# Kernel tuning notes

Measured on AMD Instinct MI355X. Metric: run time of the kernel, lower is better.

The kernel has to match this reference:

```python
import jax, jax.numpy as jnp
import numpy as np
from jax import lax

NPOINTS = 4096
K = 16
BN_EPS = 1e-5


def _fps_idx(pts, npoints):
    """Farthest point sampling indices for one cloud. pts: [N,3] -> [npoints] int32."""
    N = pts.shape[0]

    def body(carry, _):
        dist, last = carry
        d = jnp.sum((pts - pts[last]) ** 2, axis=-1)  # [N]
        dist = jnp.minimum(dist, d)
        nxt = jnp.argmax(dist).astype(jnp.int32)
        return (dist, nxt), nxt

    init = (jnp.full((N,), 1e10, pts.dtype), jnp.array(0, jnp.int32))
    _, rest = lax.scan(body, init, None, length=npoints - 1)
    return jnp.concatenate([jnp.zeros((1,), jnp.int32), rest])


def setup_inputs() -> dict:
    key = jax.random.key(0)
    k1, k2, k3 = jax.random.split(key, 3)
    B, N = 4, 16384
    P, Q = 64, 128
    return {
        "xyz": jax.random.normal(k1, (B, N, 3), jnp.float32),
        "w_planes": jax.random.normal(k2, (P, 3), jnp.float32) * 0.1,   # Conv2d(3->P,1x1,no bias)
        "w_shapes": jax.random.normal(k3, (Q, P), jnp.float32) * 0.1,   # Conv1d(P->Q,1,no bias)
        "bn_gamma": jnp.ones((Q,), jnp.float32),
        "bn_beta": jnp.zeros((Q,), jnp.float32),
        "bn_mean": jnp.zeros((Q,), jnp.float32),
        "bn_var": jnp.ones((Q,), jnp.float32),
    }


def reference(xyz, w_planes, w_shapes, bn_gamma, bn_beta, bn_mean, bn_var):
    # xyz: [B, N, 3]
    # 1) FPS -> xyz_new [B, S, 3]
    fps_idx = jax.vmap(lambda p: _fps_idx(p, NPOINTS))(xyz)            # [B, S]
    xyz_new = jnp.take_along_axis(xyz, fps_idx[:, :, None], axis=1)    # [B, S, 3]

    # 2) KNN of xyz_new in xyz (squared-L2, ascending)
    d = (jnp.sum(xyz_new ** 2, -1)[:, :, None]
         + jnp.sum(xyz ** 2, -1)[:, None, :]
         - 2.0 * jnp.einsum('bsc,bnc->bsn', xyz_new, xyz))             # [B, S, N]
    _, idx = lax.top_k(-d, K)                                          # [B, S, K], nearest first
    idx_nb = idx[:, :, 1:]                                             # drop self -> [B, S, K-1]

    # 3) group_points + center: relative neighbor coords
    knn = jax.vmap(lambda p, i: p[i])(xyz, idx_nb)                     # [B, S, K-1, 3]
    rel = knn - xyz_new[:, :, None, :]                                 # [B, S, K-1, 3]
    nrm = jnp.linalg.norm(rel, axis=-1, keepdims=True) + 1e-8          # [B, S, K-1, 1]

    # 4) 1x1 conv over coords, normalize, weighted max over neighbors
    planes = jnp.einsum('bskc,pc->bskp', rel, w_planes) / nrm          # [B, S, K-1, P]
    planes = jnp.max(nrm * planes * jnp.abs(planes), axis=2)           # [B, S, P]

    # 5) MLP: Conv1d(no bias) + BatchNorm1d(eval) + ReLU
    x = jnp.einsum('bsp,qp->bsq', planes, w_shapes)                    # [B, S, Q]
    x = (x - bn_mean) * (bn_gamma / jnp.sqrt(bn_var + BN_EPS)) + bn_beta
    shapes = jax.nn.relu(x).transpose(0, 2, 1)                         # [B, Q, S]
    return shapes, xyz_new, idx
```

## Files before the change

kernel.cpp:

```cpp
#include <hip/hip_runtime.h>

#define BB 4
#define NN 16384
#define SS 4096
#define KK 16
#define KE 17
#define PP 64
#define QQ 128

#define OFF_XYZNEW 2097152u
#define OFF_IDX    2146304u
#define OUT_ELEMS  2408448u

#define FTH 512
#define FPT (NN / FTH)
#define PAIRS (FPT / 2)
#define NWAVE (FTH / 64)

#define KTH 64
#define NBLK (SS / KTH)
#define CAP 32
#define UU  16
#define MARGIN 1e-3f

typedef float float2v __attribute__((ext_vector_type(2)));

__device__ __forceinline__ float mulrn(float a, float b) { return __fmul_rn(a, b); }
__device__ __forceinline__ float addrn(float a, float b) { return __fadd_rn(a, b); }
__device__ __forceinline__ float subrn(float a, float b) { return __fsub_rn(a, b); }

template<int CTRL>
__device__ __forceinline__ void dpp_amax(float& bv, int& bg)
{
    int vi = __builtin_amdgcn_update_dpp(__float_as_int(bv), __float_as_int(bv),
                                         CTRL, 0xf, 0xf, false);
    int gi = __builtin_amdgcn_update_dpp(bg, bg, CTRL, 0xf, 0xf, false);
    float ov = __int_as_float(vi);
    bool c = (ov > bv) | ((ov == bv) & (gi < bg));
    bg = c ? gi : bg;
    bv = c ? ov : bv;
}

__global__ __launch_bounds__(FTH)
__attribute__((amdgpu_waves_per_eu(2, 2)))
void fps_kernel(
    const float* __restrict__ xyz,
    float* __restrict__ out,
    float* __restrict__ ws, unsigned ws_floats)
{
    const int b   = blockIdx.x;
    const int tid = threadIdx.x;
    const float* base = xyz + (size_t)b * NN * 3;

    float2v pxx[PAIRS], pyy[PAIRS], pzz[PAIRS], pdd[PAIRS];
#pragma unroll
    for (int i = 0; i < PAIRS; ++i) {
        int g0 = tid + FTH * (2 * i);
        int g1 = tid + FTH * (2 * i + 1);
        pxx[i] = (float2v){ base[g0 * 3 + 0], base[g1 * 3 + 0] };
        pyy[i] = (float2v){ base[g0 * 3 + 1], base[g1 * 3 + 1] };
        pzz[i] = (float2v){ base[g0 * 3 + 2], base[g1 * 3 + 2] };
        pdd[i] = (float2v){ 1e10f, 1e10f };
        asm volatile("" : "+v"(pxx[i]));
        asm volatile("" : "+v"(pyy[i]));
        asm volatile("" : "+v"(pzz[i]));
    }

    __shared__ uint2 wvg[2][NWAVE];

    float lx = base[0], ly = base[1], lz = base[2];
    if (tid == 0) {
        unsigned o = OFF_XYZNEW + (unsigned)b * SS * 3u;
        out[o + 0] = lx; out[o + 1] = ly; out[o + 2] = lz;
        unsigned w = (unsigned)b * SS * 3u;
        if (w + 2u < ws_floats) { ws[w] = lx; ws[w + 1] = ly; ws[w + 2] = lz; }
    }

    const int lane = tid & 63;
    const int wave = tid >> 6;
    int p = 0;

    for (int s = 1; s < SS; ++s) {
#pragma clang fp contract(off)
        const float2v lx2 = (float2v){ lx, lx };
        const float2v ly2 = (float2v){ ly, ly };
        const float2v lz2 = (float2v){ lz, lz };
        float bestv = -1.0f;
        int   bestg = 0;
#pragma unroll
        for (int i = 0; i < PAIRS; ++i) {
            float2v dx = pxx[i] - lx2;
            float2v dy = pyy[i] - ly2;
            float2v dz = pzz[i] - lz2;
            float2v dd = (dx * dx + dy * dy) + dz * dz;
            float n0 = fminf(pdd[i].x, dd.x);
            float n1 = fminf(pdd[i].y, dd.y);
            pdd[i] = (float2v){ n0, n1 };
            bestg = (n0 > bestv) ? (tid + FTH * (2 * i)) : bestg;
            bestv = fmaxf(bestv, n0);
            bestg = (n1 > bestv) ? (tid + FTH * (2 * i + 1)) : bestg;
            bestv = fmaxf(bestv, n1);
        }

        dpp_amax<0x111>(bestv, bestg);
        dpp_amax<0x112>(bestv, bestg);
        dpp_amax<0x114>(bestv, bestg);
        dpp_amax<0x118>(bestv, bestg);
        dpp_amax<0x142>(bestv, bestg);
        dpp_amax<0x143>(bestv, bestg);

        if (lane == 63) wvg[p][wave] = make_uint2(__float_as_uint(bestv), (unsigned)bestg);
        __syncthreads();

        uint2 e0 = wvg[p][0];
        float bv = __uint_as_float(e0.x); int bg = (int)e0.y;
#pragma unroll
        for (int w = 1; w < NWAVE; ++w) {
            uint2 e = wvg[p][w];
            float v = __uint_as_float(e.x); int g = (int)e.y;
            bool c = (v > bv) | ((v == bv) & (g < bg));
            bg = c ? g : bg;
            bv = c ? v : bv;
        }

        int bgu = __builtin_amdgcn_readfirstlane(bg);
        lx = base[bgu * 3 + 0];
        ly = base[bgu * 3 + 1];
        lz = base[bgu * 3 + 2];

        if (tid == 0) {
            unsigned o = OFF_XYZNEW + ((unsigned)b * SS + (unsigned)s) * 3u;
            out[o + 0] = lx; out[o + 1] = ly; out[o + 2] = lz;
            unsigned w = ((unsigned)b * SS + (unsigned)s) * 3u;
            if (w + 2u < ws_floats) { ws[w] = lx; ws[w + 1] = ly; ws[w + 2] = lz; }
        }
        p ^= 1;
    }
}

__global__ __launch_bounds__(KTH) void knn_shape_kernel(
    const float* __restrict__ xyz,
    const float* __restrict__ ws, int use_ws, unsigned ws_floats,
    const float* __restrict__ w_planes, const float* __restrict__ w_shapes,
    const float* __restrict__ bn_gamma, const float* __restrict__ bn_beta,
    const float* __restrict__ bn_mean, const float* __restrict__ bn_var,
    float* __restrict__ out)
{
    __shared__ float sd[CAP][KTH];
    __shared__ int   sg[CAP][KTH];
    __shared__ float wpx[PP], wpy[PP], wpz[PP];
    __shared__ float wsh[QQ * PP];
    __shared__ float bsc[QQ], bmn[QQ], bbt[QQ];

    const int tid = threadIdx.x;
    const int blk = blockIdx.x;
    const int b   = blk / NBLK;
    const int s   = (blk % NBLK) * KTH + tid;

    for (int i = tid; i < PP; i += KTH) {
        wpx[i] = w_planes[i * 3 + 0];
        wpy[i] = w_planes[i * 3 + 1];
        wpz[i] = w_planes[i * 3 + 2];
    }
    for (int i = tid; i < QQ * PP; i += KTH) wsh[i] = w_shapes[i];
    for (int i = tid; i < QQ; i += KTH) {
        bsc[i] = bn_gamma[i] / sqrtf(bn_var[i] + 1e-5f);
        bmn[i] = bn_mean[i];
        bbt[i] = bn_beta[i];
    }
    __syncthreads();

    const float* bx = xyz + (size_t)b * NN * 3;

    float qx, qy, qz;
    {
        unsigned w = ((unsigned)b * SS + (unsigned)s) * 3u;
        if (use_ws && w + 2u < ws_floats) {
            qx = ws[w]; qy = ws[w + 1]; qz = ws[w + 2];
        } else {
            unsigned o = OFF_XYZNEW + w;
            qx = out[o + 0]; qy = out[o + 1]; qz = out[o + 2];
        }
    }
    const float  qsq   = addrn(addrn(mulrn(qx, qx), mulrn(qy, qy)), mulrn(qz, qz));
    const double qxd = (double)qx, qyd = (double)qy, qzd = (double)qz;
    const double qsq64 = qxd * qxd + qyd * qyd + qzd * qzd;

    float  kd[KE];   int ki[KE];
    double kd64[KK]; int ki64[KK];
#pragma unroll
    for (int t = 0; t < KE; ++t) { kd[t] = 3.0e38f; ki[t] = 0; }
#pragma unroll
    for (int t = 0; t < KK; ++t) { kd64[t] = 1.0e300; ki64[t] = 0; }

    int   cnt  = 0;
    float taum = 3.0e38f;

    auto drain = [&]() {
        for (int t = 0; t < CAP; ++t) {
            if (!__any(t < cnt)) break;
            const bool act = t < cnt;
            float d = 0.0f; int g = 0;
            if (act) { d = sd[t][tid]; g = sg[t][tid]; }
            if (act) {
                if (d < kd[KE - 1]) {
                    kd[KE - 1] = d; ki[KE - 1] = g;
#pragma unroll
                    for (int t2 = KE - 1; t2 >= 1; --t2) {
                        if (kd[t2] < kd[t2 - 1]) {
                            float td = kd[t2]; kd[t2] = kd[t2 - 1]; kd[t2 - 1] = td;
                            int   ti = ki[t2]; ki[t2] = ki[t2 - 1]; ki[t2 - 1] = ti;
                        }
                    }
                }
                const float* pg = bx + (size_t)g * 3u;
                float x = pg[0], y = pg[1], z = pg[2];
                double xd = (double)x, yd = (double)y, zd = (double)z;
                double tq64  = xd * xd + yd * yd + zd * zd;
                double dot64 = xd * qxd + yd * qyd + zd * qzd;
                double d64   = qsq64 + tq64 - 2.0 * dot64;
                if (d64 < kd64[KK - 1]) {
                    kd64[KK - 1] = d64; ki64[KK - 1] = g;
#pragma unroll
                    for (int t2 = KK - 1; t2 >= 1; --t2) {
                        if (kd64[t2] < kd64[t2 - 1]) {
                            double td = kd64[t2]; kd64[t2] = kd64[t2 - 1]; kd64[t2 - 1] = td;
                            int    ti = ki64[t2]; ki64[t2] = ki64[t2 - 1]; ki64[t2 - 1] = ti;
                        }
                    }
                }
            }
        }
        cnt  = 0;
        taum = kd[KE - 1] + MARGIN;
    };

    for (int g0 = 0; g0 < NN; g0 += UU) {
        float4 c4[12];
        const float4* p4 = reinterpret_cast<const float4*>(bx + (size_t)g0 * 3u);
#pragma unroll
        for (int i = 0; i < 12; ++i) c4[i] = p4[i];
        const float* cf = reinterpret_cast<const float*>(c4);
#pragma unroll
        for (int u = 0; u < UU; ++u) {
            int g = g0 + u;
            float x = cf[u * 3 + 0];
            float y = cf[u * 3 + 1];
            float z = cf[u * 3 + 2];
            float tq  = addrn(addrn(mulrn(x, x), mulrn(y, y)), mulrn(z, z));
            float dot = fmaf(z, qz, fmaf(y, qy, mulrn(x, qx)));
            float d   = subrn(addrn(qsq, tq), mulrn(2.0f, dot));
            if (d < taum) { sd[cnt][tid] = d; sg[cnt][tid] = g; ++cnt; }
        }
        if (__any(cnt > CAP - UU)) drain();
    }
    drain();

    bool agree = true;
#pragma unroll
    for (int t = 0; t < KK; ++t) agree = agree && (ki[t] == ki64[t]);

    bool hastie = false;
#pragma unroll
    for (int t = 1; t < KE; ++t) hastie = hastie || (kd[t] == kd[t - 1]);

    const bool use_f32 = agree || hastie;
    int kf[KK];
#pragma unroll
    for (int t = 0; t < KK; ++t) kf[t] = use_f32 ? ki[t] : ki64[t];

    float pl[PP];
#pragma unroll
    for (int p = 0; p < PP; ++p) pl[p] = -3.0e38f;

    for (int k = 1; k < KK; ++k) {
        int g = kf[k];
        float rx = bx[g * 3 + 0] - qx;
        float ry = bx[g * 3 + 1] - qy;
        float rz = bx[g * 3 + 2] - qz;
        float nrm  = sqrtf(rx * rx + ry * ry + rz * rz) + 1e-8f;
        float invn = 1.0f / nrm;
        for (int p = 0; p < PP; ++p) {
            float t = rx * wpx[p] + ry * wpy[p] + rz * wpz[p];
            float a = t * invn;
            float v = nrm * a * fabsf(a);
            pl[p] = fmaxf(pl[p], v);
        }
    }

    for (int q = 0; q < QQ; ++q) {
        float acc = 0.0f;
        for (int p = 0; p < PP; ++p) acc = fmaf(pl[p], wsh[q * PP + p], acc);
        float y2 = (acc - bmn[q]) * bsc[q] + bbt[q];
        y2 = fmaxf(y2, 0.0f);
        unsigned o = ((unsigned)b * QQ + (unsigned)q) * SS + (unsigned)s;
        out[o] = y2;
    }

    for (int t = 0; t < KK; ++t) {
        unsigned o = OFF_IDX + ((unsigned)b * SS + (unsigned)s) * (unsigned)KK + (unsigned)t;
        out[o] = (float)kf[t];
    }
}

extern "C" void kernel_launch(void* const* d_in, const int* in_sizes, int n_in,
                              void* d_out, int out_size, void* d_ws, size_t ws_size,
                              hipStream_t stream)
{
    const float* xyz      = (const float*)d_in[0];
    const float* w_planes = (const float*)d_in[1];
    const float* w_shapes = (const float*)d_in[2];
    const float* bn_gamma = (const float*)d_in[3];
    const float* bn_beta  = (const float*)d_in[4];
    const float* bn_mean  = (const float*)d_in[5];
    const float* bn_var   = (const float*)d_in[6];

    float* out = (float*)d_out;
    float* ws  = (float*)d_ws;

    const unsigned ws_floats = (unsigned)(ws_size / 4);
    const int use_ws = (ws_size >= (size_t)BB * SS * 3 * 4) ? 1 : 0;

    hipLaunchKernelGGL(fps_kernel, dim3(BB), dim3(FTH), 0, stream,
                       xyz, out, ws, ws_floats);

    hipLaunchKernelGGL(knn_shape_kernel, dim3(BB * NBLK), dim3(KTH), 0, stream,
                       xyz, ws, use_ws, ws_floats,
                       w_planes, w_shapes,
                       bn_gamma, bn_beta, bn_mean, bn_var,
                       out);
}
```

Baseline: 8.000 ms.

## Split KNN candidate scan across four waves per query block and merge

```diff
diff --git a/kernel.cpp b/kernel.cpp
--- a/kernel.cpp
+++ b/kernel.cpp
@@ -17,10 +17,13 @@
 #define PAIRS (FPT / 2)
 #define NWAVE (FTH / 64)
 
-#define KTH 64
-#define NBLK (SS / KTH)
-#define CAP 32
-#define UU  16
+#define KTH 256
+#define NW 4
+#define PART (NN / NW)
+#define QPB 64
+#define NBLK (SS / QPB)
+#define CAP 12
+#define UU  8
 #define MARGIN 1e-3f
 
 typedef float float2v __attribute__((ext_vector_type(2)));
@@ -149,20 +152,22 @@
     __shared__ float sd[CAP][KTH];
     __shared__ int   sg[CAP][KTH];
     __shared__ float wpx[PP], wpy[PP], wpz[PP];
-    __shared__ float wsh[QQ * PP];
     __shared__ float bsc[QQ], bmn[QQ], bbt[QQ];
-
-    const int tid = threadIdx.x;
-    const int blk = blockIdx.x;
-    const int b   = blk / NBLK;
-    const int s   = (blk % NBLK) * KTH + tid;
+    __shared__ int   ski[NW][KE][QPB];
+    __shared__ int   ski64[NW][KK][QPB];
+
+    const int tid  = threadIdx.x;
+    const int lane = tid & 63;
+    const int w    = tid >> 6;
+    const int blk  = blockIdx.x;
+    const int b    = blk / NBLK;
+    const int s    = (blk % NBLK) * QPB + lane;
 
     for (int i = tid; i < PP; i += KTH) {
         wpx[i] = w_planes[i * 3 + 0];
         wpy[i] = w_planes[i * 3 + 1];
         wpz[i] = w_planes[i * 3 + 2];
     }
-    for (int i = tid; i < QQ * PP; i += KTH) wsh[i] = w_shapes[i];
     for (int i = tid; i < QQ; i += KTH) {
         bsc[i] = bn_gamma[i] / sqrtf(bn_var[i] + 1e-5f);
         bmn[i] = bn_mean[i];
@@ -174,11 +179,11 @@
 
     float qx, qy, qz;
     {
-        unsigned w = ((unsigned)b * SS + (unsigned)s) * 3u;
-        if (use_ws && w + 2u < ws_floats) {
-            qx = ws[w]; qy = ws[w + 1]; qz = ws[w + 2];
+        unsigned wq = ((unsigned)b * SS + (unsigned)s) * 3u;
+        if (use_ws && wq + 2u < ws_floats) {
+            qx = ws[wq]; qy = ws[wq + 1]; qz = ws[wq + 2];
         } else {
-            unsigned o = OFF_XYZNEW + w;
+            unsigned o = OFF_XYZNEW + wq;
             qx = out[o + 0]; qy = out[o + 1]; qz = out[o + 2];
         }
     }
@@ -235,11 +240,12 @@
         taum = kd[KE - 1] + MARGIN;
     };
 
-    for (int g0 = 0; g0 < NN; g0 += UU) {
-        float4 c4[12];
+    const int gbeg = w * PART;
+    for (int g0 = gbeg; g0 < gbeg + PART; g0 += UU) {
+        float4 c4[6];
         const float4* p4 = reinterpret_cast<const float4*>(bx + (size_t)g0 * 3u);
 #pragma unroll
-        for (int i = 0; i < 12; ++i) c4[i] = p4[i];
+        for (int i = 0; i < 6; ++i) c4[i] = p4[i];
         const float* cf = reinterpret_cast<const float*>(c4);
 #pragma unroll
         for (int u = 0; u < UU; ++u) {
@@ -256,50 +262,124 @@
     }
     drain();
 
-    bool agree = true;
-#pragma unroll
-    for (int t = 0; t < KK; ++t) agree = agree && (ki[t] == ki64[t]);
-
-    bool hastie = false;
-#pragma unroll
-    for (int t = 1; t < KE; ++t) hastie = hastie || (kd[t] == kd[t - 1]);
-
-    const bool use_f32 = agree || hastie;
-    int kf[KK];
-#pragma unroll
-    for (int t = 0; t < KK; ++t) kf[t] = use_f32 ? ki[t] : ki64[t];
-
-    float pl[PP];
-#pragma unroll
-    for (int p = 0; p < PP; ++p) pl[p] = -3.0e38f;
-
-    for (int k = 1; k < KK; ++k) {
-        int g = kf[k];
-        float rx = bx[g * 3 + 0] - qx;
-        float ry = bx[g * 3 + 1] - qy;
-        float rz = bx[g * 3 + 2] - qz;
-        float nrm  = sqrtf(rx * rx + ry * ry + rz * rz) + 1e-8f;
-        float invn = 1.0f / nrm;
-        for (int p = 0; p < PP; ++p) {
-            float t = rx * wpx[p] + ry * wpy[p] + rz * wpz[p];
-            float a = t * invn;
-            float v = nrm * a * fabsf(a);
-            pl[p] = fmaxf(pl[p], v);
-        }
-    }
-
-    for (int q = 0; q < QQ; ++q) {
-        float acc = 0.0f;
-        for (int p = 0; p < PP; ++p) acc = fmaf(pl[p], wsh[q * PP + p], acc);
-        float y2 = (acc - bmn[q]) * bsc[q] + bbt[q];
-        y2 = fmaxf(y2, 0.0f);
-        unsigned o = ((unsigned)b * QQ + (unsigned)q) * SS + (unsigned)s;
-        out[o] = y2;
-    }
-
-    for (int t = 0; t < KK; ++t) {
-        unsigned o = OFF_IDX + ((unsigned)b * SS + (unsigned)s) * (unsigned)KK + (unsigned)t;
-        out[o] = (float)kf[t];
+#pragma unroll
+    for (int t = 0; t < KE; ++t) ski[w][t][lane] = ki[t];
+#pragma unroll
+    for (int t = 0; t < KK; ++t) ski64[w][t][lane] = ki64[t];
+    __syncthreads();
+
+    if (tid < QPB) {
+        float  kdm[KE]; int kim[KE];
+        double k64m[KK]; int i64m[KK];
+#pragma unroll
+        for (int t = 0; t < KE; ++t) { kdm[t] = 3.0e38f; kim[t] = 0; }
+#pragma unroll
+        for (int t = 0; t < KK; ++t) { k64m[t] = 1.0e300; i64m[t] = 0; }
+
+        for (int w2 = 0; w2 < NW; ++w2) {
+            int gs[KE];
+#pragma unroll
+            for (int t = 0; t < KE; ++t) gs[t] = ski[w2][t][lane];
+            for (int a = 1; a < KE; ++a) {
+                int key = gs[a]; int bi = a - 1;
+                while (bi >= 0 && gs[bi] > key) { gs[bi + 1] = gs[bi]; --bi; }
+                gs[bi + 1] = key;
+            }
+            for (int t = 0; t < KE; ++t) {
+                int g = gs[t];
+                float x = bx[g * 3 + 0];
+                float y = bx[g * 3 + 1];
+                float z = bx[g * 3 + 2];
+                float tq  = addrn(addrn(mulrn(x, x), mulrn(y, y)), mulrn(z, z));
+                float dot = fmaf(z, qz, fmaf(y, qy, mulrn(x, qx)));
+                float d   = subrn(addrn(qsq, tq), mulrn(2.0f, dot));
+                if (d < kdm[KE - 1]) {
+                    kdm[KE - 1] = d; kim[KE - 1] = g;
+#pragma unroll
+                    for (int t2 = KE - 1; t2 >= 1; --t2) {
+                        if (kdm[t2] < kdm[t2 - 1]) {
+                            float td = kdm[t2]; kdm[t2] = kdm[t2 - 1]; kdm[t2 - 1] = td;
+                            int   ti = kim[t2]; kim[t2] = kim[t2 - 1]; kim[t2 - 1] = ti;
+                        }
+                    }
+                }
+            }
+        }
+        for (int w2 = 0; w2 < NW; ++w2) {
+            int gs[KK];
+#pragma unroll
+            for (int t = 0; t < KK; ++t) gs[t] = ski64[w2][t][lane];
+            for (int a = 1; a < KK; ++a) {
+                int key = gs[a]; int bi = a - 1;
+                while (bi >= 0 && gs[bi] > key) { gs[bi + 1] = gs[bi]; --bi; }
+                gs[bi + 1] = key;
+            }
+            for (int t = 0; t < KK; ++t) {
+                int g = gs[t];
+                const float* pg = bx + (size_t)g * 3u;
+                float x = pg[0], y = pg[1], z = pg[2];
+                double xd = (double)x, yd = (double)y, zd = (double)z;
+                double tq64  = xd * xd + yd * yd + zd * zd;
+                double dot64 = xd * qxd + yd * qyd + zd * qzd;
+                double d64   = qsq64 + tq64 - 2.0 * dot64;
+                if (d64 < k64m[KK - 1]) {
+                    k64m[KK - 1] = d64; i64m[KK - 1] = g;
+#pragma unroll
+                    for (int t2 = KK - 1; t2 >= 1; --t2) {
+                        if (k64m[t2] < k64m[t2 - 1]) {
+                            double td = k64m[t2]; k64m[t2] = k64m[t2 - 1]; k64m[t2 - 1] = td;
+                            int    ti = i64m[t2]; i64m[t2] = i64m[t2 - 1]; i64m[t2 - 1] = ti;
+                        }
+                    }
+                }
+            }
+        }
+
+        bool agree = true;
+#pragma unroll
+        for (int t = 0; t < KK; ++t) agree = agree && (kim[t] == i64m[t]);
+
+        bool hastie = false;
+#pragma unroll
+        for (int t = 1; t < KE; ++t) hastie = hastie || (kdm[t] == kdm[t - 1]);
+
+        const bool use_f32 = agree || hastie;
+        int kf[KK];
+#pragma unroll
+        for (int t = 0; t < KK; ++t) kf[t] = use_f32 ? kim[t] : i64m[t];
+
+        float pl[PP];
+#pragma unroll
+        for (int p = 0; p < PP; ++p) pl[p] = -3.0e38f;
+
+        for (int k = 1; k < KK; ++k) {
+            int g = kf[k];
+            float rx = bx[g * 3 + 0] - qx;
+            float ry = bx[g * 3 + 1] - qy;
+            float rz = bx[g * 3 + 2] - qz;
+            float nrm  = sqrtf(rx * rx + ry * ry + rz * rz) + 1e-8f;
+            float invn = 1.0f / nrm;
+            for (int p = 0; p < PP; ++p) {
+                float t = rx * wpx[p] + ry * wpy[p] + rz * wpz[p];
+                float a = t * invn;
+                float v = nrm * a * fabsf(a);
+                pl[p] = fmaxf(pl[p], v);
+            }
+        }
+
+        for (int q = 0; q < QQ; ++q) {
+            float acc = 0.0f;
+            for (int p = 0; p < PP; ++p) acc = fmaf(pl[p], w_shapes[q * PP + p], acc);
+            float y2 = (acc - bmn[q]) * bsc[q] + bbt[q];
+            y2 = fmaxf(y2, 0.0f);
+            unsigned o = ((unsigned)b * QQ + (unsigned)q) * SS + (unsigned)s;
+            out[o] = y2;
+        }
+
+        for (int t = 0; t < KK; ++t) {
+            unsigned o = OFF_IDX + ((unsigned)b * SS + (unsigned)s) * (unsigned)KK + (unsigned)t;
+            out[o] = (float)kf[t];
+        }
     }
 }
 
```

After: 7.469 ms. 1.07x faster.
